# Kernel optimization log

Hardware: AMD Instinct MI355X
Metric: run time of the kernel (lower is better)

Reference implementation:

```python
import jax, jax.numpy as jnp
import numpy as np

D_MODEL, D_STATE, D_CONV, EXPAND = 768, 16, 4, 2
D_INNER = EXPAND * D_MODEL            # 1536
DT_RANK = (D_MODEL + D_STATE - 1) // D_STATE  # ceil(768/16) = 48
BATCH, L = 1024, 6


def _mamba_params(key):
    ks = jax.random.split(key, 7)
    def w(k, shape, fan_in):
        return (jax.random.normal(k, shape) / np.sqrt(fan_in)).astype(jnp.float32)
    in_proj = w(ks[0], (2 * D_INNER, D_MODEL), D_MODEL)
    conv_w = w(ks[1], (D_CONV, D_INNER), D_CONV)          # depthwise kernel, taps-major
    conv_b = (jax.random.normal(ks[2], (D_INNER,)) * 0.02).astype(jnp.float32)
    x_proj = w(ks[3], (DT_RANK + 2 * D_STATE, D_INNER), D_INNER)
    dt_w = w(ks[4], (D_INNER, DT_RANK), DT_RANK)
    dt_b = (jax.random.normal(ks[5], (D_INNER,)) * 0.1).astype(jnp.float32)
    A_log = jnp.log(jnp.tile(jnp.arange(1, D_STATE + 1, dtype=jnp.float32), (D_INNER, 1)))
    Dp = jnp.ones((D_INNER,), jnp.float32)
    out_proj = w(ks[6], (D_MODEL, D_INNER), D_INNER)
    return in_proj, conv_w, conv_b, x_proj, dt_w, dt_b, A_log, Dp, out_proj


def setup_inputs() -> dict:
    key = jax.random.key(0)
    kx, kf, kb, kg = jax.random.split(key, 4)
    f = _mamba_params(kf)
    b = _mamba_params(kb)
    names_f = ['f_in', 'f_cw', 'f_cb', 'f_xp', 'f_dtw', 'f_dtb', 'f_Alog', 'f_D', 'f_out']
    names_b = ['b_in', 'b_cw', 'b_cb', 'b_xp', 'b_dtw', 'b_dtb', 'b_Alog', 'b_D', 'b_out']
    inp = {'x': jax.random.normal(kx, (BATCH, L, D_MODEL), jnp.float32)}
    inp.update(dict(zip(names_f, f)))
    inp.update(dict(zip(names_b, b)))
    inp['ln_g'] = jnp.ones((D_MODEL,), jnp.float32)
    inp['ln_b'] = jnp.zeros((D_MODEL,), jnp.float32)
    return inp


def _causal_dwconv(x, conv_w, conv_b):
    # x: (B, L, DI); depthwise causal conv with kernel D_CONV
    Lx = x.shape[1]
    xp = jnp.pad(x, ((0, 0), (D_CONV - 1, 0), (0, 0)))
    y = sum(conv_w[k] * xp[:, k:k + Lx, :] for k in range(D_CONV))
    return y + conv_b


def _selective_scan(dt, Bm, Cm, u, A, Dp):
    # dt, u: (B, L, DI); Bm, Cm: (B, L, N); A: (DI, N)
    def step(h, inp):
        dt_t, B_t, C_t, u_t = inp                  # (B,DI), (B,N), (B,N), (B,DI)
        dA = jnp.exp(dt_t[..., None] * A)          # (B, DI, N)
        dBu = (dt_t * u_t)[..., None] * B_t[:, None, :]
        h = dA * h + dBu
        y = jnp.einsum('bdn,bn->bd', h, C_t)
        return h, y
    h0 = jnp.zeros((dt.shape[0], A.shape[0], A.shape[1]), dt.dtype)
    xs = (dt.swapaxes(0, 1), Bm.swapaxes(0, 1), Cm.swapaxes(0, 1), u.swapaxes(0, 1))
    _, ys = jax.lax.scan(step, h0, xs)
    return ys.swapaxes(0, 1) + u * Dp              # (B, L, DI)


def _mamba(x, in_proj, conv_w, conv_b, x_proj, dt_w, dt_b, A_log, Dp, out_proj):
    xz = jnp.einsum('bld,ed->ble', x, in_proj)     # (B, L, 2*DI)
    xi, z = jnp.split(xz, 2, axis=-1)
    xc = jax.nn.silu(_causal_dwconv(xi, conv_w, conv_b))
    x_dbl = jnp.einsum('bld,ed->ble', xc, x_proj)  # (B, L, R+2N)
    dt_lo, Bm, Cm = jnp.split(x_dbl, [DT_RANK, DT_RANK + D_STATE], axis=-1)
    dt = jax.nn.softplus(jnp.einsum('blr,dr->bld', dt_lo, dt_w) + dt_b)
    A = -jnp.exp(A_log)
    y = _selective_scan(dt, Bm, Cm, xc, A, Dp)
    y = y * jax.nn.silu(z)
    return jnp.einsum('bld,ed->ble', y, out_proj)


def _forward(x, f_in, f_cw, f_cb, f_xp, f_dtw, f_dtb, f_Alog, f_D, f_out,
             b_in, b_cw, b_cb, b_xp, b_dtw, b_dtb, b_Alog, b_D, b_out, ln_g, ln_b):
    x_fwd = _mamba(x, f_in, f_cw, f_cb, f_xp, f_dtw, f_dtb, f_Alog, f_D, f_out)
    x_bwd = _mamba(x[:, ::-1, :], b_in, b_cw, b_cb, b_xp, b_dtw, b_dtb, b_Alog, b_D, b_out)[:, ::-1, :]
    r = x + (x_fwd + x_bwd)                        # dropout in eval mode = identity
    mu = jnp.mean(r, axis=-1, keepdims=True)
    var = jnp.mean(jnp.square(r - mu), axis=-1, keepdims=True)
    return (r - mu) * jax.lax.rsqrt(var + 1e-5) * ln_g + ln_b


def reference(x, f_in, f_cw, f_cb, f_xp, f_dtw, f_dtb, f_Alog, f_D, f_out,
              b_in, b_cw, b_cb, b_xp, b_dtw, b_dtb, b_Alog, b_D, b_out, ln_g, ln_b):
    return _forward(x, f_in, f_cw, f_cb, f_xp, f_dtw, f_dtb, f_Alog, f_D, f_out,
                    b_in, b_cw, b_cb, b_xp, b_dtw, b_dtb, b_Alog, b_D, b_out, ln_g, ln_b)
```

## Files before the change

### kernel.cpp

```cpp
#include <hip/hip_runtime.h>
#include <hip/hip_bf16.h>


typedef __bf16 bf16x8 __attribute__((ext_vector_type(8)));
typedef __bf16 bf16x2 __attribute__((ext_vector_type(2)));
typedef float  f32x4  __attribute__((ext_vector_type(4)));

#define M_ROWS   6144
#define DMODEL   768
#define DINNER   1536
#define NSTATE   16
#define LSEQ     6
#define NB_BATCH 1024
#define N_XZ     6144
#define DT_RANK  48

__global__ __launch_bounds__(256) void prep_kernel(
    const float* __restrict__ x, const float* __restrict__ f_in, const float* __restrict__ b_in,
    const float* __restrict__ fxp, const float* __restrict__ bxp,
    const float* __restrict__ fdtw, const float* __restrict__ bdtw,
    const float* __restrict__ fout, const float* __restrict__ bout,
    __hip_bfloat16* __restrict__ x_bf, __hip_bfloat16* __restrict__ w1,
    __hip_bfloat16* __restrict__ w2, __hip_bfloat16* __restrict__ dtw,
    __hip_bfloat16* __restrict__ wout) {
    const int NX = M_ROWS * DMODEL;
    const int NW = 2 * DINNER * DMODEL;
    const int N2 = 2 * 128 * DINNER;
    const int ND = 2 * DINNER * 64;
    int i = blockIdx.x * 256 + threadIdx.x;
    if (i < NX) { x_bf[i] = __float2bfloat16(x[i]); return; }
    i -= NX;
    if (i < NW) { w1[i] = __float2bfloat16(f_in[i]); return; }
    i -= NW;
    if (i < NW) { w1[NW + i] = __float2bfloat16(b_in[i]); return; }
    i -= NW;
    if (i < N2) {
        int c = i % DINNER, r = (i / DINNER) % 128, dir = i / (128 * DINNER);
        const float* xp = dir ? bxp : fxp;
        w2[i] = __float2bfloat16(r < 80 ? xp[r * DINNER + c] : 0.f);
        return;
    }
    i -= N2;
    if (i < ND) {
        int j = i % 64, d = (i / 64) % DINNER, dir = i / (64 * DINNER);
        const float* w = dir ? bdtw : fdtw;
        dtw[i] = __float2bfloat16(j < DT_RANK ? w[d * DT_RANK + j] : 0.f);
        return;
    }
    i -= ND;
    if (i < NW) {
        int c = i % (2 * DINNER), r = i / (2 * DINNER);
        float v = (c < DINNER) ? fout[r * DINNER + c] : bout[r * DINNER + (c - DINNER)];
        wout[i] = __float2bfloat16(v);
    }
}

template <int TM, int OUTMODE, bool NPART>
__global__ __launch_bounds__(256, (TM >= 256 ? 2 : 4)) void gemm_bt_kernel(
    const __hip_bfloat16* __restrict__ A, int lda,
    const __hip_bfloat16* __restrict__ W, int ldw, int Nw,
    void* __restrict__ Cout, int ldc, int K,
    float* __restrict__ bcout,
    int nTiles, int mTiles,
    size_t az, size_t wz, size_t cz) {
    constexpr int MI  = TM / 32;
    constexpr int ACH = (TM >= 64) ? TM / 64 : 1;
    __shared__ __align__(16) __hip_bfloat16 As[TM * 32];
    __shared__ __align__(16) __hip_bfloat16 Ws[128 * 32];

    const int L = blockIdx.x;
    int nb, mi, zi;
    if (NPART) {
        const int nChunk = nTiles >> 3;
        const int t = L >> 3;
        nb = (L & 7) * nChunk + (t % nChunk);
        const int g = t / nChunk;
        mi = g % mTiles;  zi = g / mTiles;
    } else {
        const int t = L >> 3;
        const int g = (t / nTiles) * 8 + (L & 7);
        nb = t % nTiles;
        mi = g % mTiles;  zi = g / mTiles;
    }

    A += (size_t)zi * az;
    W += (size_t)zi * wz;

    const int tid  = threadIdx.x;
    const int bm   = mi * TM;
    const int bn   = nb * 128;
    const int wave = tid >> 6;
    const int lane = tid & 63;
    const int wm   = (wave >> 1) * (TM / 2);
    const int wn   = (wave & 1) * 64;
    const int lrow = lane & 15;
    const int kg   = lane >> 4;
    const int sw8  = ((((lrow >> 1) & 3) ^ kg) << 3);

    const __hip_bfloat16* aptr[ACH];
    #pragma unroll
    for (int c = 0; c < ACH; ++c) {
        int chunk = tid + c * 256;
        int row   = chunk >> 2;
        int seg   = (((chunk & 3) ^ ((row >> 1) & 3)) << 3);
        aptr[c] = &A[(size_t)(bm + row) * lda + seg];
    }
    const __hip_bfloat16* wptr[2];
    #pragma unroll
    for (int c = 0; c < 2; ++c) {
        int chunk = tid + c * 256;
        int row   = chunk >> 2;
        int seg   = (((chunk & 3) ^ ((row >> 1) & 3)) << 3);
        wptr[c] = &W[(size_t)(bn + row) * ldw + seg];
    }

    f32x4 acc[MI][4] = {};

    for (int k0 = 0; k0 < K; k0 += 32) {
        #pragma unroll
        for (int c = 0; c < ACH; ++c)
            __builtin_amdgcn_global_load_lds(
                (const __attribute__((address_space(1))) void*)(aptr[c] + k0),
                (__attribute__((address_space(3))) void*)&As[(tid + c * 256) * 8], 16, 0, 0);
        #pragma unroll
        for (int c = 0; c < 2; ++c)
            __builtin_amdgcn_global_load_lds(
                (const __attribute__((address_space(1))) void*)(wptr[c] + k0),
                (__attribute__((address_space(3))) void*)&Ws[(tid + c * 256) * 8], 16, 0, 0);
        __syncthreads();

        bf16x8 af[MI], wf[4];
        #pragma unroll
        for (int i = 0; i < MI; ++i)
            af[i] = *(const bf16x8*)&As[(wm + i * 16 + lrow) * 32 + sw8];
        #pragma unroll
        for (int j = 0; j < 4; ++j)
            wf[j] = *(const bf16x8*)&Ws[(wn + j * 16 + lrow) * 32 + sw8];
        #pragma unroll
        for (int i = 0; i < MI; ++i)
            #pragma unroll
            for (int j = 0; j < 4; ++j)
                acc[i][j] = __builtin_amdgcn_mfma_f32_16x16x32_bf16(af[i], wf[j], acc[i][j], 0, 0, 0);
        __syncthreads();
    }

    const int rbase = kg * 4;
    #pragma unroll
    for (int i = 0; i < MI; ++i) {
        #pragma unroll
        for (int j = 0; j < 4; ++j) {
            int col = bn + wn + j * 16 + lrow;
            if (col < Nw) {
                #pragma unroll
                for (int r = 0; r < 4; ++r) {
                    int row = bm + wm + i * 16 + rbase + r;
                    if (OUTMODE == 3) {
                        if (col < DT_RANK)
                            ((__hip_bfloat16*)Cout)[(size_t)row * 128 + zi * 64 + col]
                                = __float2bfloat16(acc[i][j][r]);
                        else if (col < 80)
                            bcout[(size_t)row * 64 + zi * 32 + (col - DT_RANK)] = acc[i][j][r];
                        else
                            ((__hip_bfloat16*)Cout)[(size_t)row * 128 + zi * 64 + (col - 32)]
                                = __float2bfloat16(0.f);
                    } else if (OUTMODE == 1) {
                        ((__hip_bfloat16*)Cout)[(size_t)zi * cz + (size_t)row * ldc + col]
                            = __float2bfloat16(acc[i][j][r]);
                    } else {
                        ((float*)Cout)[(size_t)zi * cz + (size_t)row * ldc + col] = acc[i][j][r];
                    }
                }
            }
        }
    }
}

__global__ __launch_bounds__(256) void conv_silu_kernel(
    const __hip_bfloat16* __restrict__ xz,
    const float* __restrict__ fcw, const float* __restrict__ fcb,
    const float* __restrict__ bcw, const float* __restrict__ bcb,
    __hip_bfloat16* __restrict__ xc) {
    const int NG = DINNER / 8;
    int idx = blockIdx.x * 256 + threadIdx.x;
    if (idx >= NB_BATCH * 2 * NG) return;
    int g   = idx % NG;
    int t   = idx / NG;
    int dir = t & 1;
    int b   = t >> 1;
    int c8  = g * 8;

    const float* cw = dir ? bcw : fcw;
    const float* cb = dir ? bcb : fcb;
    float w[4][8], bias[8];
    #pragma unroll
    for (int k = 0; k < 4; ++k)
        #pragma unroll
        for (int j = 0; j < 8; ++j) w[k][j] = cw[k * DINNER + c8 + j];
    #pragma unroll
    for (int j = 0; j < 8; ++j) bias[j] = cb[c8 + j];

    float xv[6][8];
    #pragma unroll
    for (int l = 0; l < 6; ++l) {
        bf16x8 v = *(const bf16x8*)&xz[(size_t)(b * 6 + l) * N_XZ + (size_t)dir * (2 * DINNER) + c8];
        #pragma unroll
        for (int j = 0; j < 8; ++j) xv[l][j] = (float)v[j];
    }

    #pragma unroll
    for (int l = 0; l < 6; ++l) {
        float acc[8];
        #pragma unroll
        for (int j = 0; j < 8; ++j) acc[j] = bias[j];
        if (dir == 0) {
            #pragma unroll
            for (int k = 0; k < 4; ++k) {
                int ll = l - 3 + k;
                if (ll >= 0)
                    #pragma unroll
                    for (int j = 0; j < 8; ++j) acc[j] += w[k][j] * xv[ll][j];
            }
        } else {
            #pragma unroll
            for (int k = 0; k < 4; ++k) {
                int ll = l + 3 - k;
                if (ll < 6)
                    #pragma unroll
                    for (int j = 0; j < 8; ++j) acc[j] += w[k][j] * xv[ll][j];
            }
        }
        bf16x8 o;
        #pragma unroll
        for (int j = 0; j < 8; ++j) {
            float y = acc[j] * __builtin_amdgcn_rcpf(1.f + __expf(-acc[j]));
            o[j] = (__bf16)y;
        }
        *(bf16x8*)&xc[(size_t)(b * 6 + l) * (2 * DINNER) + (size_t)dir * DINNER + c8] = o;
    }
}

template <bool BWD>
__device__ __forceinline__ void scan_body(
    size_t o3,
    size_t oz,
    size_t obc,
    const __hip_bfloat16* __restrict__ dtb_buf, const float* __restrict__ bc,
    const __hip_bfloat16* __restrict__ xc, const __hip_bfloat16* __restrict__ xz,
    float dtb0, float dtb1, float Dp0, float Dp1, float Av00, float Av01,
    __hip_bfloat16* __restrict__ yg) {
    float h0[NSTATE], h1[NSTATE];
    #pragma unroll
    for (int n = 0; n < NSTATE; ++n) { h0[n] = 0.f; h1[n] = 0.f; }

    #pragma unroll
    for (int s = 0; s < LSEQ; ++s) {
        const int rr = BWD ? (LSEQ - 1 - s) : s;
        const size_t r3  = o3  + (size_t)rr * (2 * DINNER);
        const size_t rz  = oz  + (size_t)rr * N_XZ;
        const float* bcr = bc + obc + (size_t)rr * 64;

        bf16x2 dtv = *(const bf16x2*)&dtb_buf[r3];
        bf16x2 uv  = *(const bf16x2*)&xc[r3];
        bf16x2 zv  = *(const bf16x2*)&xz[rz];

        float dtp0 = (float)dtv[0] + dtb0;
        float dtp1 = (float)dtv[1] + dtb1;
        float dt0  = (dtp0 > 20.f) ? dtp0 : __logf(1.f + __expf(dtp0));
        float dt1  = (dtp1 > 20.f) ? dtp1 : __logf(1.f + __expf(dtp1));
        float u0   = (float)uv[0], u1 = (float)uv[1];
        float du0  = dt0 * u0,     du1 = dt1 * u1;
        float e0   = __expf(dt0 * Av00);
        float e1   = __expf(dt1 * Av01);

        float p0 = 1.f, p1 = 1.f, y0 = 0.f, y1 = 0.f;
        #pragma unroll
        for (int q = 0; q < 4; ++q) {
            float4 B4 = *(const float4*)(bcr + 4 * q);
            float4 C4 = *(const float4*)(bcr + NSTATE + 4 * q);
            p0 *= e0; h0[4*q+0] = p0 * h0[4*q+0] + du0 * B4.x; y0 += h0[4*q+0] * C4.x;
            p1 *= e1; h1[4*q+0] = p1 * h1[4*q+0] + du1 * B4.x; y1 += h1[4*q+0] * C4.x;
            p0 *= e0; h0[4*q+1] = p0 * h0[4*q+1] + du0 * B4.y; y0 += h0[4*q+1] * C4.y;
            p1 *= e1; h1[4*q+1] = p1 * h1[4*q+1] + du1 * B4.y; y1 += h1[4*q+1] * C4.y;
            p0 *= e0; h0[4*q+2] = p0 * h0[4*q+2] + du0 * B4.z; y0 += h0[4*q+2] * C4.z;
            p1 *= e1; h1[4*q+2] = p1 * h1[4*q+2] + du1 * B4.z; y1 += h1[4*q+2] * C4.z;
            p0 *= e0; h0[4*q+3] = p0 * h0[4*q+3] + du0 * B4.w; y0 += h0[4*q+3] * C4.w;
            p1 *= e1; h1[4*q+3] = p1 * h1[4*q+3] + du1 * B4.w; y1 += h1[4*q+3] * C4.w;
        }
        float z0 = (float)zv[0], z1 = (float)zv[1];
        float g0 = z0 * __builtin_amdgcn_rcpf(1.f + __expf(-z0));
        float g1 = z1 * __builtin_amdgcn_rcpf(1.f + __expf(-z1));
        bf16x2 o;
        o[0] = (__bf16)((y0 + u0 * Dp0) * g0);
        o[1] = (__bf16)((y1 + u1 * Dp1) * g1);
        *(bf16x2*)&yg[r3] = o;
    }
}

__global__ __launch_bounds__(256) void scan_kernel(
    const __hip_bfloat16* __restrict__ dtb_buf, const float* __restrict__ bc,
    const __hip_bfloat16* __restrict__ xc, const __hip_bfloat16* __restrict__ xz,
    const float* __restrict__ fAlog, const float* __restrict__ fdtb, const float* __restrict__ fD,
    const float* __restrict__ bAlog, const float* __restrict__ bdtb, const float* __restrict__ bD,
    __hip_bfloat16* __restrict__ yg) {
    const int NP = DINNER / 2;
    int idx = blockIdx.x * 256 + threadIdx.x;
    if (idx >= NB_BATCH * 2 * NP) return;
    int dp  = idx % NP;
    int t2  = idx / NP;
    int dir = t2 & 1;
    int b   = t2 >> 1;
    int d   = dp * 2;

    const float* dtbv = dir ? bdtb : fdtb;
    const float* Dv   = dir ? bD   : fD;
    const float* Al   = dir ? bAlog : fAlog;
    float dtb0 = dtbv[d],     dtb1 = dtbv[d + 1];
    float Dp0  = Dv[d],       Dp1  = Dv[d + 1];
    float Av00 = -__expf(Al[d * NSTATE]);
    float Av01 = -__expf(Al[(d + 1) * NSTATE]);

    size_t o3  = (size_t)(b * LSEQ) * (2 * DINNER) + (size_t)dir * DINNER + d;
    size_t oz  = (size_t)(b * LSEQ) * N_XZ + (size_t)dir * (2 * DINNER) + DINNER + d;
    size_t obc = (size_t)(b * LSEQ) * 64 + dir * 32;

    if (dir == 0)
        scan_body<false>(o3, oz, obc, dtb_buf, bc, xc, xz,
                         dtb0, dtb1, Dp0, Dp1, Av00, Av01, yg);
    else
        scan_body<true>(o3, oz, obc, dtb_buf, bc, xc, xz,
                        dtb0, dtb1, Dp0, Dp1, Av00, Av01, yg);
}

__global__ __launch_bounds__(256) void ln_kernel(
    const float* __restrict__ x, const float* __restrict__ pp,
    float* __restrict__ out,
    const float* __restrict__ g, const float* __restrict__ bta) {
    const size_t PZ = (size_t)M_ROWS * DMODEL;
    int row = blockIdx.x;
    const float* xr = x  + (size_t)row * DMODEL;
    const float* p0 = pp + (size_t)row * DMODEL;
    const float* p1 = p0 + PZ;
    float* orow = out + (size_t)row * DMODEL;
    float v[3], s = 0.f, ss = 0.f;
    #pragma unroll
    for (int i = 0; i < 3; ++i) {
        int c = threadIdx.x + i * 256;
        v[i] = xr[c] + p0[c] + p1[c];
        s += v[i]; ss += v[i] * v[i];
    }
    #pragma unroll
    for (int off = 32; off > 0; off >>= 1) {
        s  += __shfl_down(s, off);
        ss += __shfl_down(ss, off);
    }
    __shared__ float sh[8];
    int wave = threadIdx.x >> 6, lane = threadIdx.x & 63;
    if (lane == 0) { sh[wave] = s; sh[4 + wave] = ss; }
    __syncthreads();
    if (threadIdx.x == 0) {
        sh[0] = sh[0] + sh[1] + sh[2] + sh[3];
        sh[4] = sh[4] + sh[5] + sh[6] + sh[7];
    }
    __syncthreads();
    float mu  = sh[0] * (1.f / DMODEL);
    float var = sh[4] * (1.f / DMODEL) - mu * mu;
    float rs  = rsqrtf(var + 1e-5f);
    #pragma unroll
    for (int i = 0; i < 3; ++i) {
        int c = threadIdx.x + i * 256;
        orow[c] = (v[i] - mu) * rs * g[c] + bta[c];
    }
}

extern "C" void kernel_launch(void* const* d_in, const int* in_sizes, int n_in,
                              void* d_out, int out_size, void* d_ws, size_t ws_size,
                              hipStream_t stream) {
    const float* x     = (const float*)d_in[0];
    const float* f_in  = (const float*)d_in[1];
    const float* f_cw  = (const float*)d_in[2];
    const float* f_cb  = (const float*)d_in[3];
    const float* f_xp  = (const float*)d_in[4];
    const float* f_dtw = (const float*)d_in[5];
    const float* f_dtb = (const float*)d_in[6];
    const float* f_Al  = (const float*)d_in[7];
    const float* f_D   = (const float*)d_in[8];
    const float* f_out = (const float*)d_in[9];
    const float* b_in  = (const float*)d_in[10];
    const float* b_cw  = (const float*)d_in[11];
    const float* b_cb  = (const float*)d_in[12];
    const float* b_xp  = (const float*)d_in[13];
    const float* b_dtw = (const float*)d_in[14];
    const float* b_dtb = (const float*)d_in[15];
    const float* b_Al  = (const float*)d_in[16];
    const float* b_D   = (const float*)d_in[17];
    const float* b_out = (const float*)d_in[18];
    const float* ln_g  = (const float*)d_in[19];
    const float* ln_b  = (const float*)d_in[20];

    char* ws = (char*)d_ws;
    size_t off = 0;
    auto alloc = [&](size_t bytes) { char* p = ws + off; off += (bytes + 255) & ~(size_t)255; return p; };
    __hip_bfloat16* x_bf   = (__hip_bfloat16*)alloc((size_t)M_ROWS * DMODEL * 2);
    __hip_bfloat16* w1_bf  = (__hip_bfloat16*)alloc((size_t)N_XZ * DMODEL * 2);
    __hip_bfloat16* w2     = (__hip_bfloat16*)alloc((size_t)2 * 128 * DINNER * 2);
    __hip_bfloat16* dtw_bf = (__hip_bfloat16*)alloc((size_t)2 * DINNER * 64 * 2);
    __hip_bfloat16* wout   = (__hip_bfloat16*)alloc((size_t)DMODEL * 2 * DINNER * 2);
    __hip_bfloat16* xz_bf  = (__hip_bfloat16*)alloc((size_t)M_ROWS * N_XZ * 2);
    __hip_bfloat16* xc_bf  = (__hip_bfloat16*)alloc((size_t)M_ROWS * 2 * DINNER * 2);
    __hip_bfloat16* dtlo   = (__hip_bfloat16*)alloc((size_t)M_ROWS * 128 * 2);
    float*          bcbuf  = (float*)alloc((size_t)M_ROWS * 64 * 4);
    __hip_bfloat16* dt_bf  = (__hip_bfloat16*)alloc((size_t)M_ROWS * 2 * DINNER * 2);
    __hip_bfloat16* yg_bf  = (__hip_bfloat16*)alloc((size_t)M_ROWS * 2 * DINNER * 2);
    float*          pp     = (float*)alloc((size_t)2 * M_ROWS * DMODEL * 4);
    (void)ws_size;

    {
        int n = M_ROWS * DMODEL + 3 * (2 * DINNER * DMODEL) + 2 * 128 * DINNER + 2 * DINNER * 64;
        prep_kernel<<<(n + 255) / 256, 256, 0, stream>>>(
            x, f_in, b_in, f_xp, b_xp, f_dtw, b_dtw, f_out, b_out,
            x_bf, w1_bf, w2, dtw_bf, wout);
    }

    {
        int nT = N_XZ / 128, mT = M_ROWS / 128;
        gemm_bt_kernel<128, 1, true><<<nT * mT, 256, 0, stream>>>(
            x_bf, DMODEL, w1_bf, DMODEL, N_XZ,
            (void*)xz_bf, N_XZ, DMODEL, nullptr, nT, mT, 0, 0, 0);
    }

    {
        int n = NB_BATCH * 2 * (DINNER / 8);
        conv_silu_kernel<<<(n + 255) / 256, 256, 0, stream>>>(xz_bf, f_cw, f_cb, b_cw, b_cb, xc_bf);
    }

    {
        int nT = 1, mT = M_ROWS / 64;
        gemm_bt_kernel<64, 3, false><<<nT * mT * 2, 256, 0, stream>>>(
            xc_bf, 2 * DINNER, w2, DINNER, 96,
            (void*)dtlo, 0, DINNER, bcbuf, nT, mT,
            (size_t)DINNER, (size_t)128 * DINNER, 0);
    }

    {
        int nT = DINNER / 128, mT = M_ROWS / 128;
        gemm_bt_kernel<128, 1, false><<<nT * mT * 2, 256, 0, stream>>>(
            dtlo, 128, dtw_bf, 64, DINNER,
            (void*)dt_bf, 2 * DINNER, 64, nullptr, nT, mT,
            (size_t)64, (size_t)DINNER * 64, (size_t)DINNER);
    }

    {
        int n = NB_BATCH * 2 * (DINNER / 2);
        scan_kernel<<<(n + 255) / 256, 256, 0, stream>>>(dt_bf, bcbuf, xc_bf, xz_bf,
                                                         f_Al, f_dtb, f_D,
                                                         b_Al, b_dtb, b_D, yg_bf);
    }

    {
        int nT = DMODEL / 128, mT = M_ROWS / 64;
        gemm_bt_kernel<64, 0, false><<<nT * mT * 2, 256, 0, stream>>>(
            yg_bf, 2 * DINNER, wout, 2 * DINNER, DMODEL,
            (void*)pp, DMODEL, DINNER, nullptr, nT, mT,
            (size_t)DINNER, (size_t)DINNER, (size_t)M_ROWS * DMODEL);
    }

    ln_kernel<<<M_ROWS, 256, 0, stream>>>(x, pp, (float*)d_out, ln_g, ln_b);
}
```

Baseline: 399.5 us.

## Replace in_proj GEMM with 256x192-tile, 4-stage direct-to-LDS pipelined kernel

Adds a dedicated kernel for the first (in_proj) GEMM. It uses 512 threads, 256x192 output tiles and a 4-buffer LDS ring filled by global_load_lds with an XOR swizzle, keeping two stages of loads in flight. It also raises wave priority around the MFMA block, and the grid mapping groups N tiles for L2 reuse. The goal is to hide global-load latency and cut LDS traffic per MFMA compared with the generic 128x128 kernel. The cost is hand-tuned vmcnt waits tied to this exact shape, plus higher LDS and register use per block.

```diff
diff --git a/kernel.cpp b/kernel.cpp
--- a/kernel.cpp
+++ b/kernel.cpp
@@ -55,6 +55,130 @@
     }
 }
 
+__global__ __launch_bounds__(512, 2) void gemm1_pipe_kernel(
+    const __hip_bfloat16* __restrict__ A,
+    const __hip_bfloat16* __restrict__ W,
+    __hip_bfloat16* __restrict__ C) {
+    __shared__ __align__(16) __hip_bfloat16 lds[4][14336];
+
+    const int L  = blockIdx.x;
+    const int tq = L >> 3;
+    const int nb = (L & 7) * 4 + (tq & 3);
+    const int mi = tq >> 2;
+    const int bm = mi * 256;
+    const int bn = nb * 192;
+
+    const int tid  = threadIdx.x;
+    const int wave = tid >> 6;
+    const int lane = tid & 63;
+    const int lrow = lane & 15;
+    const int kg   = lane >> 4;
+    const int sw8  = ((((lrow >> 1) & 3) ^ kg) << 3);
+    const int wm   = (wave >> 2) * 128;
+    const int wn   = (wave & 3) * 48;
+    const bool w03 = (tid < 256);
+
+    const __hip_bfloat16* srcA0;
+    const __hip_bfloat16* srcA1;
+    const __hip_bfloat16* srcB0;
+    const __hip_bfloat16* srcB1;
+    {
+        int ch  = tid;
+        int row = ch >> 2;
+        int seg = (((ch & 3) ^ ((row >> 1) & 3)) << 3);
+        srcA0 = A + (size_t)(bm + row) * DMODEL + seg;
+        ch  = 512 + tid;
+        row = ch >> 2;
+        seg = (((ch & 3) ^ ((row >> 1) & 3)) << 3);
+        srcA1 = A + (size_t)(bm + row) * DMODEL + seg;
+        ch  = tid;
+        row = ch >> 2;
+        seg = (((ch & 3) ^ ((row >> 1) & 3)) << 3);
+        srcB0 = W + (size_t)(bn + row) * DMODEL + seg;
+        ch  = 512 + tid;
+        row = ch >> 2;
+        seg = (((ch & 3) ^ ((row >> 1) & 3)) << 3);
+        srcB1 = W + (size_t)(bn + row) * DMODEL + seg;
+    }
+    const int dst0 = tid * 8;
+    const int dst1 = 4096 + tid * 8;
+    const int dst2 = 8192 + tid * 8;
+    const int dst3 = 12288 + tid * 8;
+
+    auto stage = [&](int t) {
+        const int ko = t * 32;
+        __hip_bfloat16* d = &lds[t & 3][0];
+        __builtin_amdgcn_global_load_lds(
+            (const __attribute__((address_space(1))) void*)(srcA0 + ko),
+            (__attribute__((address_space(3))) void*)(d + dst0), 16, 0, 0);
+        __builtin_amdgcn_global_load_lds(
+            (const __attribute__((address_space(1))) void*)(srcA1 + ko),
+            (__attribute__((address_space(3))) void*)(d + dst1), 16, 0, 0);
+        __builtin_amdgcn_global_load_lds(
+            (const __attribute__((address_space(1))) void*)(srcB0 + ko),
+            (__attribute__((address_space(3))) void*)(d + dst2), 16, 0, 0);
+        if (w03)
+            __builtin_amdgcn_global_load_lds(
+                (const __attribute__((address_space(1))) void*)(srcB1 + ko),
+                (__attribute__((address_space(3))) void*)(d + dst3), 16, 0, 0);
+    };
+
+    stage(0);
+    stage(1);
+    if (w03) asm volatile("s_waitcnt vmcnt(4)" ::: "memory");
+    else     asm volatile("s_waitcnt vmcnt(3)" ::: "memory");
+    __builtin_amdgcn_s_barrier();
+    asm volatile("" ::: "memory");
+
+    f32x4 acc[8][3] = {};
+
+    for (int t = 0; t < 24; ++t) {
+        const __hip_bfloat16* buf = &lds[t & 3][0];
+
+        bf16x8 wf[3], af[8];
+        #pragma unroll
+        for (int j = 0; j < 3; ++j)
+            wf[j] = *(const bf16x8*)&buf[8192 + (wn + j * 16 + lrow) * 32 + sw8];
+        #pragma unroll
+        for (int i = 0; i < 8; ++i)
+            af[i] = *(const bf16x8*)&buf[(wm + i * 16 + lrow) * 32 + sw8];
+
+        if (t < 22) stage(t + 2);
+
+        __builtin_amdgcn_s_setprio(1);
+        #pragma unroll
+        for (int i = 0; i < 8; ++i)
+            #pragma unroll
+            for (int j = 0; j < 3; ++j)
+                acc[i][j] = __builtin_amdgcn_mfma_f32_16x16x32_bf16(af[i], wf[j], acc[i][j], 0, 0, 0);
+        __builtin_amdgcn_s_setprio(0);
+
+        if (t < 22) {
+            if (w03) asm volatile("s_waitcnt vmcnt(4)" ::: "memory");
+            else     asm volatile("s_waitcnt vmcnt(3)" ::: "memory");
+            __builtin_amdgcn_s_barrier();
+            asm volatile("" ::: "memory");
+        } else if (t == 22) {
+            asm volatile("s_waitcnt vmcnt(0)" ::: "memory");
+            __builtin_amdgcn_s_barrier();
+            asm volatile("" ::: "memory");
+        }
+    }
+
+    #pragma unroll
+    for (int i = 0; i < 8; ++i) {
+        #pragma unroll
+        for (int j = 0; j < 3; ++j) {
+            const int col = bn + wn + j * 16 + lrow;
+            #pragma unroll
+            for (int r = 0; r < 4; ++r) {
+                const int row = bm + wm + i * 16 + kg * 4 + r;
+                C[(size_t)row * N_XZ + col] = __float2bfloat16(acc[i][j][r]);
+            }
+        }
+    }
+}
+
 template <int TM, int OUTMODE, bool NPART>
 __global__ __launch_bounds__(256, (TM >= 256 ? 2 : 4)) void gemm_bt_kernel(
     const __hip_bfloat16* __restrict__ A, int lda,
@@ -421,12 +545,7 @@
             x_bf, w1_bf, w2, dtw_bf, wout);
     }
 
-    {
-        int nT = N_XZ / 128, mT = M_ROWS / 128;
-        gemm_bt_kernel<128, 1, true><<<nT * mT, 256, 0, stream>>>(
-            x_bf, DMODEL, w1_bf, DMODEL, N_XZ,
-            (void*)xz_bf, N_XZ, DMODEL, nullptr, nT, mT, 0, 0, 0);
-    }
+    gemm1_pipe_kernel<<<768, 512, 0, stream>>>(x_bf, w1_bf, xz_bf);
 
     {
         int n = NB_BATCH * 2 * (DINNER / 8);
```

New measurement: 376.5 us. 5.7% less time.
